# Kernel optimization log

Hardware: AMD Instinct MI355X
Metric: run time of the kernel (lower is better)

Reference implementation:

```python
import jax, jax.numpy as jnp
import numpy as np

B, S, HID, NH, K = 4, 1500, 1024, 16, 64
DH = HID // NH  # 64


def _rel_bias(pos_emb, length):
    # pos_emb: [2K+1, d]; Shaw-style relative position embedding lookup -> [S, S, d]
    kk = (pos_emb.shape[0] - 1) // 2
    idx = jnp.arange(length)
    dist = jnp.clip(idx[None, :] - idx[:, None], -kk, kk) + kk
    return pos_emb[dist]


def setup_inputs() -> dict:
    key = jax.random.key(0)
    ks = jax.random.split(key, 12)
    sq = 1.0 / np.sqrt(HID)
    inp = {
        "query": jax.random.normal(ks[0], (B, S, HID), jnp.float32),
        "key": jax.random.normal(ks[1], (B, S, HID), jnp.float32),
        "value": jax.random.normal(ks[2], (B, S, HID), jnp.float32),
        # per-head QKV projections stacked over heads: [NH, HID, DH]
        "Wq": jax.random.normal(ks[3], (NH, HID, DH), jnp.float32) * sq,
        "bq": jnp.zeros((NH, DH), jnp.float32),
        "Wk": jax.random.normal(ks[4], (NH, HID, DH), jnp.float32) * sq,
        "bk": jnp.zeros((NH, DH), jnp.float32),
        "Wv": jax.random.normal(ks[5], (NH, HID, DH), jnp.float32) * sq,
        "bv": jnp.zeros((NH, DH), jnp.float32),
        # relative position tables [2K+1, DH]
        "pos_k": jax.random.normal(ks[6], (2 * K + 1, DH), jnp.float32) * 0.1,
        "pos_v": jax.random.normal(ks[7], (2 * K + 1, DH), jnp.float32) * 0.1,
        # output projection
        "W_fc": jax.random.normal(ks[8], (HID, HID), jnp.float32) * sq,
        "b_fc": jnp.zeros((HID,), jnp.float32),
    }
    return inp


def reference(query, key, value, Wq, bq, Wk, bk, Wv, bv, pos_k, pos_v, W_fc, b_fc):
    seq = query.shape[1]
    k_bias = _rel_bias(pos_k, seq)  # [S, S, DH]
    v_bias = _rel_bias(pos_v, seq)  # [S, S, DH]

    # batched per-head projections: [B, NH, S, DH]
    q = jnp.einsum('bsh,nhd->bnsd', query, Wq) + bq[None, :, None, :]
    k = jnp.einsum('bsh,nhd->bnsd', key, Wk) + bk[None, :, None, :]
    v = jnp.einsum('bsh,nhd->bnsd', value, Wv) + bv[None, :, None, :]

    attn_1 = jnp.einsum('bnqd,bnkd->bnqk', q, k)
    attn_2 = jnp.einsum('bnqd,qkd->bnqk', q, k_bias)  # Shaw relative key bias
    scores = (attn_1 + attn_2) / jnp.sqrt(jnp.float32(DH))
    w = jax.nn.softmax(scores, axis=-1)  # [B, NH, S, S]

    values_1 = jnp.einsum('bnqk,bnkd->bnqd', w, v)
    values_2 = jnp.einsum('bnqk,qkd->bnqd', w, v_bias)  # Shaw relative value bias
    heads = values_1 + values_2  # [B, NH, S, DH]

    # concat heads in head order -> [B, S, HID]
    hidden = jnp.transpose(heads, (0, 2, 1, 3)).reshape(query.shape[0], seq, -1)
    return hidden @ W_fc + b_fc
```

## Files before the change

### kernel.cpp

```cpp
#include <hip/hip_runtime.h>
#include <stdint.h>

typedef unsigned short u16;
typedef __attribute__((ext_vector_type(8))) short bf16x8;
typedef __attribute__((ext_vector_type(4))) float f32x4;

#define MFMA16(a, b, c) __builtin_amdgcn_mfma_f32_16x16x32_bf16(a, b, c, 0, 0, 0)

__device__ __forceinline__ u16 f2bf(float x) {
  union { float f; uint32_t u; } v; v.f = x;
  uint32_t r = (v.u + 0x7FFFu + ((v.u >> 16) & 1u)) >> 16;
  return (u16)r;
}
__device__ __forceinline__ float bf2f(u16 h) {
  union { uint32_t u; float f; } v; v.u = ((uint32_t)h) << 16; return v.f;
}
__device__ __forceinline__ uint cvt_pk_bf16(float a, float b) {
  uint r;
  asm("v_cvt_pk_bf16_f32 %0, %1, %2" : "=v"(r) : "v"(a), "v"(b));
  return r;
}
__device__ __forceinline__ void gll16(const void* g, void* s) {
  __builtin_amdgcn_global_load_lds((const __attribute__((address_space(1))) unsigned int*)g,
                                   (__attribute__((address_space(3))) unsigned int*)s, 16, 0, 0);
}


__global__ __launch_bounds__(256) void pack_w_kernel(const float* __restrict__ Wq,
                                                     const float* __restrict__ Wk,
                                                     const float* __restrict__ Wv,
                                                     const float* __restrict__ Wfc,
                                                     const float* __restrict__ bq,
                                                     const float* __restrict__ bk,
                                                     const float* __restrict__ bv,
                                                     const float* __restrict__ posk,
                                                     const float* __restrict__ posv,
                                                     u16* __restrict__ Wt,
                                                     u16* __restrict__ Wfct,
                                                     float* __restrict__ biascat,
                                                     u16* __restrict__ poskbf,
                                                     u16* __restrict__ posvT) {
  __shared__ float tile[64][65];
  const int bi = blockIdx.x;
  if (bi == 1024) {
    for (int i = threadIdx.x; i < 1024; i += 256) {
      biascat[i] = bq[i]; biascat[1024 + i] = bk[i]; biascat[2048 + i] = bv[i];
    }
    for (int i = threadIdx.x; i < 144 * 64; i += 256) {
      int r = i >> 6;
      poskbf[i] = (r < 129) ? f2bf(posk[i]) : (u16)0;
    }
    const int d = threadIdx.x & 63, rr = threadIdx.x >> 6;
#pragma unroll
    for (int j = 0; j < 34; ++j) {
      const int r = rr * 34 + j;
      posvT[d * 136 + r] = (r < 129) ? f2bf(posv[(size_t)r * 64 + d]) : (u16)0;
    }
    return;
  }
  const int r = threadIdx.x >> 2, c0 = (threadIdx.x & 3) * 16;
  const float* src;
  u16* outp;
  if (bi < 768) {
    const int z = bi >> 8, rem = bi & 255, n = rem >> 4, h0 = (rem & 15) * 64;
    const float* W = z == 0 ? Wq : (z == 1 ? Wk : Wv);
    src = W + (size_t)n * 65536 + (size_t)(h0 + r) * 64 + c0;
    outp = Wt + (size_t)z * (1024UL * 1024UL) + (size_t)(n * 64 + r) * 1024 + h0 + c0;
  } else {
    const int t = bi - 768;
    const int i0 = (t & 15) * 64, o0 = (t >> 4) * 64;
    src = Wfc + (size_t)(i0 + r) * 1024 + o0 + c0;
    outp = Wfct + (size_t)(o0 + r) * 1024 + i0 + c0;
  }
#pragma unroll
  for (int j = 0; j < 16; j += 4) {
    float4 f = *(const float4*)(src + j);
    tile[r][c0 + j] = f.x; tile[r][c0 + j + 1] = f.y;
    tile[r][c0 + j + 2] = f.z; tile[r][c0 + j + 3] = f.w;
  }
  __syncthreads();
#pragma unroll
  for (int j = 0; j < 16; ++j) outp[j] = f2bf(tile[c0 + j][r]);
}

__global__ __launch_bounds__(256, 4) void gemm_bt_kernel(
    const float* __restrict__ aQ, const float* __restrict__ aK, const float* __restrict__ aV,
    const u16* __restrict__ Ahid,
    const u16* __restrict__ Bbase, long bStride,
    const float* __restrict__ biasBase, long biasStride,
    u16* __restrict__ outBF, u16* __restrict__ VtOut, float* __restrict__ outF, int mode) {
  __shared__ u16 smem[17408];

  const int nwg = 376 * gridDim.z;
  const int cpx = nwg >> 3;
  const int lid = blockIdx.x + (blockIdx.y << 3) + blockIdx.z * 376;
  const int swz = (lid & 7) * cpx + (lid >> 3);
  const int z = swz / 376;
  const int rem = swz - z * 376;
  const int m0 = (rem >> 3) * 128, n0 = (rem & 7) * 128;

  const u16* Bt = Bbase + (size_t)z * bStride;
  const float* bias = biasBase + (size_t)z * biasStride;
  const int tid = threadIdx.x, w = tid >> 6, lane = tid & 63;
  const int quad = lane >> 4, l16 = lane & 15;
  const int wm = w >> 1, wn = w & 1;
  const int srow = w * 16 + (lane >> 2);
  const int scol = (lane & 3) * 8;

  const u16* gB0 = Bt + (size_t)(n0 + srow) * 1024 + scol;
  const u16* gB1 = gB0 + 64UL * 1024;
  const int slab = (w * 16) * 32;

  f32x4 acc[4][4];
  const f32x4 zf = {0.f, 0.f, 0.f, 0.f};
#pragma unroll
  for (int a = 0; a < 4; ++a)
#pragma unroll
    for (int b = 0; b < 4; ++b) acc[a][b] = zf;

  auto gllB = [&](int buf) {
    gll16(gB0, &smem[8192 + buf * 4096 + slab]);
    gll16(gB1, &smem[8192 + buf * 4096 + slab + 64 * 32]);
    gB0 += 32; gB1 += 32;
  };
  auto compute = [&](int buf) {
    bf16x8 af[4], bfr[4];
#pragma unroll
    for (int f = 0; f < 4; ++f) {
      af[f]  = *(const bf16x8*)&smem[buf * 4096 + (wm * 64 + f * 16 + l16) * 32 + quad * 8];
      bfr[f] = *(const bf16x8*)&smem[8192 + buf * 4096 + (wn * 64 + f * 16 + l16) * 32 + quad * 8];
    }
#pragma unroll
    for (int fm = 0; fm < 4; ++fm)
#pragma unroll
      for (int fn = 0; fn < 4; ++fn)
        acc[fm][fn] = MFMA16(af[fm], bfr[fn], acc[fm][fn]);
  };

  if (mode == 0) {
    const float* srcF = z == 0 ? aQ : (z == 1 ? aK : aV);
    int rowA0 = m0 + srow;        if (rowA0 > 5999) rowA0 = 5999;
    int rowA1 = m0 + 64 + srow;   if (rowA1 > 5999) rowA1 = 5999;
    const float* fA0 = srcF + (size_t)rowA0 * 1024 + scol;
    const float* fA1 = srcF + (size_t)rowA1 * 1024 + scol;
    float4 a00, a01, a10, a11;
    auto loadA = [&]() {
      a00 = *(const float4*)fA0; a01 = *(const float4*)(fA0 + 4);
      a10 = *(const float4*)fA1; a11 = *(const float4*)(fA1 + 4);
      fA0 += 32; fA1 += 32;
    };
    const int adst = (w * 16 + (lane >> 2)) * 32 + (lane & 3) * 8;
    auto dswriteA = [&](int buf) {
      uint4 lo, hi;
      lo.x = cvt_pk_bf16(a00.x, a00.y); lo.y = cvt_pk_bf16(a00.z, a00.w);
      lo.z = cvt_pk_bf16(a01.x, a01.y); lo.w = cvt_pk_bf16(a01.z, a01.w);
      hi.x = cvt_pk_bf16(a10.x, a10.y); hi.y = cvt_pk_bf16(a10.z, a10.w);
      hi.z = cvt_pk_bf16(a11.x, a11.y); hi.w = cvt_pk_bf16(a11.z, a11.w);
      *(uint4*)&smem[buf * 4096 + adst] = lo;
      *(uint4*)&smem[buf * 4096 + adst + 64 * 32] = hi;
    };

    loadA();
    gllB(0);

#define QKV_SYNC(BUF) do {                                    \
      asm volatile("s_waitcnt vmcnt(0)" ::: "memory");        \
      __builtin_amdgcn_sched_barrier(0);                      \
      dswriteA(BUF);                                          \
      asm volatile("s_waitcnt lgkmcnt(0)" ::: "memory");      \
      __builtin_amdgcn_sched_barrier(0);                      \
      __builtin_amdgcn_s_barrier();                           \
      __builtin_amdgcn_sched_barrier(0);                      \
    } while (0)

#pragma unroll 1
    for (int pr = 0; pr < 16; ++pr) {
      QKV_SYNC(0);
      loadA(); gllB(1);
      compute(0);
      QKV_SYNC(1);
      if (pr < 15) { loadA(); gllB(0); }
      compute(1);
    }
#undef QKV_SYNC

    if (z < 2) {
      const float scale = (z == 0) ? 0.125f : 1.0f;
      u16* out = outBF + (size_t)z * (4UL * 16 * 1536 * 64);
#pragma unroll
      for (int fm = 0; fm < 4; ++fm) {
#pragma unroll
        for (int i = 0; i < 4; ++i) {
          const int m = m0 + wm * 64 + fm * 16 + quad * 4 + i;
          if (m >= 6000) continue;
          const int bb = m / 1500;
          const int s = m - bb * 1500;
#pragma unroll
          for (int fn = 0; fn < 4; ++fn) {
            const int n = n0 + wn * 64 + fn * 16 + l16;
            const float vv = (acc[fm][fn][i] + bias[n]) * scale;
            const int h = n >> 6, d = n & 63;
            out[((size_t)(bb * 16 + h) * 1536 + s) * 64 + d] = f2bf(vv);
          }
        }
      }
    } else {
      __syncthreads();
      u16* T = smem;
#pragma unroll
      for (int fm = 0; fm < 4; ++fm) {
        const int ml = wm * 64 + fm * 16 + quad * 4;
#pragma unroll
        for (int fn = 0; fn < 4; ++fn) {
          const int nl = wn * 64 + fn * 16 + l16;
          const float b0 = bias[n0 + nl];
          uint2 pk;
          pk.x = cvt_pk_bf16(acc[fm][fn][0] + b0, acc[fm][fn][1] + b0);
          pk.y = cvt_pk_bf16(acc[fm][fn][2] + b0, acc[fm][fn][3] + b0);
          *(uint2*)&T[nl * 136 + ml] = pk;
        }
      }
      __syncthreads();
#pragma unroll 1
      for (int ps = 0; ps < 8; ++ps) {
        const int row = ps * 16 + (tid >> 4);
        const int col = (tid & 15) * 8;
        const int ng = n0 + row;
        const int h = ng >> 6, d = ng & 63;
        const int mg = m0 + col;
        uint4 v = *(const uint4*)&T[row * 136 + col];
        const int bb0 = mg / 1500, bb7 = (mg + 7) / 1500;
        if ((bb0 == bb7) & (mg + 7 < 6000)) {
          u16* dst = VtOut + ((size_t)((bb0 * 16 + h) * 64 + d)) * 1536 + (mg - bb0 * 1500);
          uint2 loh; loh.x = v.x; loh.y = v.y;
          uint2 hih; hih.x = v.z; hih.y = v.w;
          *(uint2*)dst = loh;
          *(uint2*)(dst + 4) = hih;
        } else {
          const u16* tv = (const u16*)&v;
#pragma unroll
          for (int j = 0; j < 8; ++j) {
            const int m = mg + j;
            if (m < 6000) {
              const int bb = m / 1500;
              VtOut[((size_t)((bb * 16 + h) * 64 + d)) * 1536 + (m - bb * 1500)] = tv[j];
            }
          }
        }
      }
    }
  } else {
    const u16* gA0 = Ahid + (size_t)(m0 + srow) * 1024 + scol;
    const u16* gA1 = gA0 + 64UL * 1024;
    auto stage1 = [&](int buf) {
      gll16(gA0, &smem[buf * 4096 + slab]);
      gll16(gA1, &smem[buf * 4096 + slab + 64 * 32]);
      gA0 += 32; gA1 += 32;
      gllB(buf);
    };
    stage1(0);
#define FC_SYNC() do {                                        \
      asm volatile("s_waitcnt vmcnt(0)" ::: "memory");        \
      __builtin_amdgcn_sched_barrier(0);                      \
      __builtin_amdgcn_s_barrier();                           \
      __builtin_amdgcn_sched_barrier(0);                      \
    } while (0)
#pragma unroll 1
    for (int pr = 0; pr < 16; ++pr) {
      FC_SYNC();
      stage1(1);
      compute(0);
      FC_SYNC();
      if (pr < 15) stage1(0);
      compute(1);
    }
#undef FC_SYNC
#pragma unroll
    for (int fm = 0; fm < 4; ++fm) {
#pragma unroll
      for (int i = 0; i < 4; ++i) {
        const int m = m0 + wm * 64 + fm * 16 + quad * 4 + i;
        if (m >= 6000) continue;
#pragma unroll
        for (int fn = 0; fn < 4; ++fn) {
          const int n = n0 + wn * 64 + fn * 16 + l16;
          outF[(size_t)m * 1024 + n] = acc[fm][fn][i] + bias[n];
        }
      }
    }
  }
}

__global__ __launch_bounds__(256, 4) void attn_kernel(const u16* __restrict__ qkv,
                                                      const u16* __restrict__ Vt,
                                                      const u16* __restrict__ poskbf,
                                                      const u16* __restrict__ posvT,
                                                      const float* __restrict__ posv,
                                                      u16* __restrict__ hidden) {
  const size_t ZS = 4UL * 16 * 1536 * 64;
  __shared__ u16 qb_s[64 * 136];
  __shared__ u16 kbuf[2][2048];
  __shared__ u16 vbuf[2][2048];

  const int tid = threadIdx.x;
  const int w = tid >> 6, lane = tid & 63, quad = lane >> 4, l16 = lane & 15;
  const int bi = blockIdx.x;
  const int bh = bi & 63;
  const int q0 = (bi >> 6) * 64, qw0 = q0 + w * 16;
  const int b = bh >> 4;
  const size_t sb = (size_t)bh * (1536UL * 64UL);
  const u16* Qp = qkv + sb;
  const u16* Kp = qkv + ZS + sb;
  const u16* Vtb = Vt + (size_t)bh * (64UL * 1536UL);
  u16* qb_row = qb_s + (w * 16 + l16) * 136;

  const int r8 = lane >> 3, c8 = lane & 7;
  const int vr = lane >> 2, vc = lane & 3;
  const int kprow = ((( (w * 8 + r8) & 15) >> 2) * 8) + (((w * 8 + r8) >> 4) * 4) + ((w * 8 + r8) & 3);
  const u16* kSrc = Kp + (size_t)kprow * 64 + ((c8 ^ r8) * 8);
  const u16* vSrc = Vtb + (size_t)(w * 16 + vr) * 1536 + ((vc ^ ((vr >> 1) & 3)) * 8);
  u16* const kDst = &kbuf[0][0] + w * 512;
  u16* const vDst = &vbuf[0][0] + w * 512;

  gll16(kSrc, kDst);
  gll16(vSrc, vDst);

  const u16* qptr = Qp + (size_t)(qw0 + l16) * 64 + quad * 8;
  const bf16x8 qB0 = *(const bf16x8*)qptr;
  const bf16x8 qB1 = *(const bf16x8*)(qptr + 32);

  const f32x4 zf = {0.f, 0.f, 0.f, 0.f};
#pragma unroll
  for (int nf = 0; nf < 9; ++nf) {
    const u16* bp = poskbf + (size_t)(nf * 16 + l16) * 64 + quad * 8;
    bf16x8 b0 = *(const bf16x8*)bp;
    bf16x8 b1 = *(const bf16x8*)(bp + 32);
    f32x4 c = zf;
    c = MFMA16(qB0, b0, c);
    c = MFMA16(qB1, b1, c);
    const int col = nf * 16 + l16;
    if (col < 136) {
#pragma unroll
      for (int i = 0; i < 4; ++i)
        qb_s[(w * 16 + quad * 4 + i) * 136 + col] = f2bf(c[i]);
    }
  }
  __syncthreads();

  const float L2E = 1.44269504f;
  const float M8 = -8.0f * L2E;
  const float eLow  = __builtin_fmaf(bf2f(qb_row[0]), L2E, M8);
  const float eHigh = __builtin_fmaf(bf2f(qb_row[128]), L2E, M8);

  f32x4 accf[4];
#pragma unroll
  for (int dc = 0; dc < 4; ++dc) accf[dc] = zf;
  float sSimple = 0.f, sLowSave = 0.f, sDall = 0.f, sD0 = 0.f, sD128 = 0.f;

  const int itLowEnd = (qw0 >= 95) ? (((qw0 - 95) >> 5) + 1) : 0;
  const int itHigh0 = (qw0 + 110) >> 5;
  const int dEnd = itHigh0 < 46 ? itHigh0 : 46;

  const int kswz = (quad ^ (l16 & 7)) * 8;
  const int kswz4 = ((quad + 4) ^ (l16 & 7)) * 8;
  const int vpos = (quad ^ ((l16 >> 1) & 3)) * 8;

  const u16* kS = kSrc + 2048;
  const u16* vS = vSrc + 32;

  auto body = [&](int it, const u16* kb, const u16* vbse, bool doStage, int stageOff) {
    if (doStage) {
      gll16(kS, kDst + stageOff);
      gll16(vS, vDst + stageOff);
      kS += 2048; vS += 32;
    }

    if (it == itLowEnd) sLowSave = sSimple;
    const int phase = (it < itLowEnd) ? 0 : ((it >= 46) ? 1 : ((it < dEnd) ? 1 : 2));

    bf16x8 ka00 = *(const bf16x8*)(kb + l16 * 64 + kswz);
    bf16x8 ka01 = *(const bf16x8*)(kb + l16 * 64 + kswz4);
    bf16x8 ka10 = *(const bf16x8*)(kb + (16 + l16) * 64 + kswz);
    bf16x8 ka11 = *(const bf16x8*)(kb + (16 + l16) * 64 + kswz4);
    bf16x8 vb0 = *(const bf16x8*)(vbse + l16 * 32 + vpos);
    bf16x8 vb1 = *(const bf16x8*)(vbse + (16 + l16) * 32 + vpos);
    bf16x8 vb2 = *(const bf16x8*)(vbse + (32 + l16) * 32 + vpos);
    bf16x8 vb3 = *(const bf16x8*)(vbse + (48 + l16) * 32 + vpos);

    float qb[2][4];
    if (phase == 1) {
      const int base = it * 32 + 64 - qw0 - l16 + quad * 8;
#pragma unroll
      for (int cg = 0; cg < 2; ++cg) {
#pragma unroll
        for (int i = 0; i < 4; ++i) {
          int delta = base + cg * 4 + i;
          delta = delta < 0 ? 0 : (delta > 128 ? 128 : delta);
          qb[cg][i] = bf2f(qb_row[delta]);
        }
      }
    }

    f32x4 cc[2];
    cc[0] = zf; cc[1] = zf;
    cc[0] = MFMA16(ka00, qB0, cc[0]);
    cc[0] = MFMA16(ka01, qB1, cc[0]);
    cc[1] = MFMA16(ka10, qB0, cc[1]);
    cc[1] = MFMA16(ka11, qB1, cc[1]);

    float pvv[2][4];
    if (phase != 1) {
      const float eB = (phase == 0) ? eLow : eHigh;
#pragma unroll
      for (int cg = 0; cg < 2; ++cg) {
#pragma unroll
        for (int i = 0; i < 4; ++i) {
          float p = __builtin_amdgcn_exp2f(__builtin_fmaf(cc[cg][i], L2E, eB));
          sSimple += p; pvv[cg][i] = p;
        }
      }
    } else {
      const int kc0 = it * 32;
#pragma unroll
      for (int cg = 0; cg < 2; ++cg) {
        const int krow0 = kc0 + quad * 8 + cg * 4;
        const int dbase = krow0 + 64 - qw0 - l16;
#pragma unroll
        for (int i = 0; i < 4; ++i) {
          int delta = dbase + i;
          delta = delta < 0 ? 0 : (delta > 128 ? 128 : delta);
          const float t = cc[cg][i] + qb[cg][i];
          float p = __builtin_amdgcn_exp2f(__builtin_fmaf(t, L2E, M8));
          if (krow0 + i >= 1500) p = 0.f;
          sDall += p;
          sD0   += (delta == 0)   ? p : 0.f;
          sD128 += (delta == 128) ? p : 0.f;
          pvv[cg][i] = p;
        }
        const uint pk01 = cvt_pk_bf16(pvv[cg][0], pvv[cg][1]);
        const uint pk23 = cvt_pk_bf16(pvv[cg][2], pvv[cg][3]);
        const u16 hb[4] = {(u16)pk01, (u16)(pk01 >> 16), (u16)pk23, (u16)(pk23 >> 16)};
#pragma unroll
        for (int i = 0; i < 4; ++i) {
          int delta = dbase + i;
          delta = delta < 0 ? 0 : (delta > 128 ? 128 : delta);
          if ((delta != 0) & (delta != 128)) qb_row[delta] = hb[i];
        }
      }
    }

    union { uint u[4]; bf16x8 v; } pa;
    pa.u[0] = cvt_pk_bf16(pvv[0][0], pvv[0][1]);
    pa.u[1] = cvt_pk_bf16(pvv[0][2], pvv[0][3]);
    pa.u[2] = cvt_pk_bf16(pvv[1][0], pvv[1][1]);
    pa.u[3] = cvt_pk_bf16(pvv[1][2], pvv[1][3]);

    accf[0] = MFMA16(pa.v, vb0, accf[0]);
    accf[1] = MFMA16(pa.v, vb1, accf[1]);
    accf[2] = MFMA16(pa.v, vb2, accf[2]);
    accf[3] = MFMA16(pa.v, vb3, accf[3]);

    __syncthreads();
  };

#pragma unroll 1
  for (int pr = 0; pr < 23; ++pr) {
    const int it0 = pr * 2;
    body(it0,     &kbuf[0][0], &vbuf[0][0], true, 2048);
    body(it0 + 1, &kbuf[1][0], &vbuf[1][0], true, 0);
  }
  body(46, &kbuf[0][0], &vbuf[0][0], false, 0);

  const float sLow = sLowSave;
  const float sHigh = sSimple - sLowSave;
  float lpart = sSimple + sDall;
  float clow = sLow + sD0;
  float chigh = sHigh + sD128;
#pragma unroll
  for (int m = 16; m <= 32; m <<= 1) {
    lpart += __shfl_xor(lpart, m);
    clow  += __shfl_xor(clow, m);
    chigh += __shfl_xor(chigh, m);
  }
  const float linv = 1.0f / lpart;

  {
    const int qg_row = qw0 + l16;
    if (quad == 0) qb_row[0] = 0;
    const int lim = 64 - qg_row;
    for (int d = 1 + quad; d < lim; d += 4) qb_row[d] = 0;
    const int dlo = 1564 - qg_row;
    for (int d = dlo + quad; d <= 127; d += 4) qb_row[d] = 0;
  }

  f32x4 o2[4];
#pragma unroll
  for (int dc = 0; dc < 4; ++dc) o2[dc] = zf;
#pragma unroll
  for (int kk = 0; kk < 4; ++kk) {
    bf16x8 pa2 = *(const bf16x8*)(qb_row + kk * 32 + quad * 8);
#pragma unroll
    for (int dc = 0; dc < 4; ++dc) {
      bf16x8 vb2r = *(const bf16x8*)(posvT + (size_t)(dc * 16 + l16) * 136 + kk * 32 + quad * 8);
      o2[dc] = MFMA16(pa2, vb2r, o2[dc]);
    }
  }

  float li[4], cl[4], ch[4];
#pragma unroll
  for (int i = 0; i < 4; ++i) {
    const int srcl = quad * 4 + i;
    li[i] = __shfl(linv, srcl);
    cl[i] = __shfl(clow, srcl);
    ch[i] = __shfl(chigh, srcl);
  }

#pragma unroll
  for (int dc = 0; dc < 4; ++dc) {
    const int d = dc * 16 + l16;
    const float pv0 = posv[d], pv1 = posv[128 * 64 + d];
#pragma unroll
    for (int i = 0; i < 4; ++i) {
      const int qg = qw0 + quad * 4 + i;
      if (qg < 1500) {
        const float val = (accf[dc][i] + o2[dc][i] + cl[i] * pv0 + ch[i] * pv1) * li[i];
        hidden[((size_t)(b * 1500 + qg)) * 1024 + (bh & 15) * 64 + d] = f2bf(val);
      }
    }
  }
}

extern "C" void kernel_launch(void* const* d_in, const int* in_sizes, int n_in,
                              void* d_out, int out_size, void* d_ws, size_t ws_size,
                              hipStream_t stream) {
  const float* query = (const float*)d_in[0];
  const float* key   = (const float*)d_in[1];
  const float* value = (const float*)d_in[2];
  const float* Wq = (const float*)d_in[3];
  const float* bq = (const float*)d_in[4];
  const float* Wk = (const float*)d_in[5];
  const float* bk = (const float*)d_in[6];
  const float* Wv = (const float*)d_in[7];
  const float* bv = (const float*)d_in[8];
  const float* posk = (const float*)d_in[9];
  const float* posv = (const float*)d_in[10];
  const float* Wfc = (const float*)d_in[11];
  const float* bfc = (const float*)d_in[12];
  float* out = (float*)d_out;

  char* p = (char*)d_ws;
  u16* X = (u16*)p;        p += 3UL * 6016 * 1024 * 2;
  u16* Wt = (u16*)p;       p += 3UL * 1024 * 1024 * 2;
  u16* Wfct = (u16*)p;     p += 1024UL * 1024 * 2;
  u16* poskbf = (u16*)p;   p += 144UL * 64 * 2;
  u16* posvT = (u16*)p;    p += 64UL * 136 * 2;
  float* biascat = (float*)p; p += 3UL * 1024 * 4;
  u16* qkv = (u16*)p;      p += 3UL * 4 * 16 * 1536 * 64 * 2;
  u16* hidden = X;
  u16* Vt = X + 6291456;

  pack_w_kernel<<<dim3(1025), 256, 0, stream>>>(Wq, Wk, Wv, Wfc, bq, bk, bv, posk, posv,
                                                Wt, Wfct, biascat, poskbf, posvT);

  gemm_bt_kernel<<<dim3(8, 47, 3), 256, 0, stream>>>(
      query, key, value, nullptr, Wt, 1024L * 1024, biascat, 1024L, qkv, Vt, nullptr, 0);

  attn_kernel<<<dim3(1536), 256, 0, stream>>>(qkv, Vt, poskbf, posvT, posv, hidden);

  gemm_bt_kernel<<<dim3(8, 47, 1), 256, 0, stream>>>(
      nullptr, nullptr, nullptr, hidden, Wfct, 0L, bfc, 0L, nullptr, nullptr, out, 1);
}
```

Measured before the change: 348.4 us.

## Prefetch QKV activation tiles two stages ahead with partial vmcnt waits

The QKV projection GEMM loop now keeps two sets of fp32 A-tile registers. Global loads are issued one extra stage ahead, and the code waits with partial s_waitcnt vmcnt counts instead of draining all loads before each LDS write. The bf16 conversion and LDS write for the next buffer move to just after the barrier, so they overlap with the in-flight B loads and the MFMA compute. The cost is more register pressure and fragile hand-counted vmcnt values that depend on how many loads gllB issues.

```diff
diff --git a/kernel.cpp b/kernel.cpp
--- a/kernel.cpp
+++ b/kernel.cpp
@@ -143,46 +143,61 @@
     int rowA1 = m0 + 64 + srow;   if (rowA1 > 5999) rowA1 = 5999;
     const float* fA0 = srcF + (size_t)rowA0 * 1024 + scol;
     const float* fA1 = srcF + (size_t)rowA1 * 1024 + scol;
-    float4 a00, a01, a10, a11;
-    auto loadA = [&]() {
-      a00 = *(const float4*)fA0; a01 = *(const float4*)(fA0 + 4);
-      a10 = *(const float4*)fA1; a11 = *(const float4*)(fA1 + 4);
+    float4 s0a, s0b, s0c, s0d, s1a, s1b, s1c, s1d;
+    auto loadA0 = [&]() {
+      s0a = *(const float4*)fA0; s0b = *(const float4*)(fA0 + 4);
+      s0c = *(const float4*)fA1; s0d = *(const float4*)(fA1 + 4);
+      fA0 += 32; fA1 += 32;
+    };
+    auto loadA1 = [&]() {
+      s1a = *(const float4*)fA0; s1b = *(const float4*)(fA0 + 4);
+      s1c = *(const float4*)fA1; s1d = *(const float4*)(fA1 + 4);
       fA0 += 32; fA1 += 32;
     };
     const int adst = (w * 16 + (lane >> 2)) * 32 + (lane & 3) * 8;
-    auto dswriteA = [&](int buf) {
+    auto wrA = [&](int buf, float4 A0, float4 A1, float4 A2, float4 A3) {
       uint4 lo, hi;
-      lo.x = cvt_pk_bf16(a00.x, a00.y); lo.y = cvt_pk_bf16(a00.z, a00.w);
-      lo.z = cvt_pk_bf16(a01.x, a01.y); lo.w = cvt_pk_bf16(a01.z, a01.w);
-      hi.x = cvt_pk_bf16(a10.x, a10.y); hi.y = cvt_pk_bf16(a10.z, a10.w);
-      hi.z = cvt_pk_bf16(a11.x, a11.y); hi.w = cvt_pk_bf16(a11.z, a11.w);
+      lo.x = cvt_pk_bf16(A0.x, A0.y); lo.y = cvt_pk_bf16(A0.z, A0.w);
+      lo.z = cvt_pk_bf16(A1.x, A1.y); lo.w = cvt_pk_bf16(A1.z, A1.w);
+      hi.x = cvt_pk_bf16(A2.x, A2.y); hi.y = cvt_pk_bf16(A2.z, A2.w);
+      hi.z = cvt_pk_bf16(A3.x, A3.y); hi.w = cvt_pk_bf16(A3.z, A3.w);
       *(uint4*)&smem[buf * 4096 + adst] = lo;
       *(uint4*)&smem[buf * 4096 + adst + 64 * 32] = hi;
     };
 
-    loadA();
+    loadA0();
     gllB(0);
-
-#define QKV_SYNC(BUF) do {                                    \
-      asm volatile("s_waitcnt vmcnt(0)" ::: "memory");        \
-      __builtin_amdgcn_sched_barrier(0);                      \
-      dswriteA(BUF);                                          \
-      asm volatile("s_waitcnt lgkmcnt(0)" ::: "memory");      \
-      __builtin_amdgcn_sched_barrier(0);                      \
-      __builtin_amdgcn_s_barrier();                           \
-      __builtin_amdgcn_sched_barrier(0);                      \
-    } while (0)
+    loadA1();
+    asm volatile("s_waitcnt vmcnt(10)" ::: "memory");
+    __builtin_amdgcn_sched_barrier(0);
+    wrA(0, s0a, s0b, s0c, s0d);
+    loadA0();
 
 #pragma unroll 1
     for (int pr = 0; pr < 16; ++pr) {
-      QKV_SYNC(0);
-      loadA(); gllB(1);
+      if (pr < 15) { asm volatile("s_waitcnt vmcnt(8)" ::: "memory"); }
+      else         { asm volatile("s_waitcnt vmcnt(0)" ::: "memory"); }
+      asm volatile("s_waitcnt lgkmcnt(0)" ::: "memory");
+      __builtin_amdgcn_sched_barrier(0);
+      __builtin_amdgcn_s_barrier();
+      __builtin_amdgcn_sched_barrier(0);
+      wrA(1, s1a, s1b, s1c, s1d);
+      gllB(1);
+      if (pr < 15) loadA1();
       compute(0);
-      QKV_SYNC(1);
-      if (pr < 15) { loadA(); gllB(0); }
+      if (pr < 15) { asm volatile("s_waitcnt vmcnt(8)" ::: "memory"); }
+      else         { asm volatile("s_waitcnt vmcnt(0)" ::: "memory"); }
+      asm volatile("s_waitcnt lgkmcnt(0)" ::: "memory");
+      __builtin_amdgcn_sched_barrier(0);
+      __builtin_amdgcn_s_barrier();
+      __builtin_amdgcn_sched_barrier(0);
+      if (pr < 15) {
+        wrA(0, s0a, s0b, s0c, s0d);
+        gllB(0);
+      }
+      if (pr < 14) loadA0();
       compute(1);
     }
-#undef QKV_SYNC
 
     if (z < 2) {
       const float scale = (z == 0) ? 0.125f : 1.0f;
```

Result: slower. 372.6 us (+7.0%).
